# Performance work log

Measured on AMD Instinct MI355X. Metric: run time of the kernel, lower is better.

The kernel has to match this reference:

```python
import jax, jax.numpy as jnp
import numpy as np

H = 512
IN = 64
OUT = 1


def _lstm_layer(x, W_ih, W_hh, b_ih, b_hh):
    # x: (B, T, D). PyTorch gate order: i, f, g, o stacked along 4H.
    B, T, _ = x.shape
    Hd = W_hh.shape[1]
    # Precompute input contribution for all timesteps (one big GEMM).
    xg = jnp.einsum('btd,gd->btg', x, W_ih) + b_ih + b_hh  # (B, T, 4H)

    def step(carry, xg_t):
        h, c = carry
        gates = xg_t + h @ W_hh.T  # (B, 4H)
        i, f, g, o = jnp.split(gates, 4, axis=-1)
        i = jax.nn.sigmoid(i)
        f = jax.nn.sigmoid(f)
        g = jnp.tanh(g)
        o = jax.nn.sigmoid(o)
        c = f * c + i * g
        h = o * jnp.tanh(c)
        return (h, c), h

    h0 = jnp.zeros((B, Hd), x.dtype)
    c0 = jnp.zeros((B, Hd), x.dtype)
    (_, _), hs = jax.lax.scan(step, (h0, c0), jnp.swapaxes(xg, 0, 1))
    return jnp.swapaxes(hs, 0, 1)  # (B, T, H)


def setup_inputs() -> dict:
    key = jax.random.key(0)
    ks = jax.random.split(key, 12)
    s = 1.0 / np.sqrt(H)  # PyTorch LSTM init scale
    u = lambda k, shp: jax.random.uniform(k, shp, jnp.float32, -s, s)
    return {
        'x': jax.random.normal(ks[0], (64, 512, IN), jnp.float32),
        'W_ih0': u(ks[1], (4 * H, IN)),
        'W_hh0': u(ks[2], (4 * H, H)),
        'b_ih0': u(ks[3], (4 * H,)),
        'b_hh0': u(ks[4], (4 * H,)),
        'W_ih1': u(ks[5], (4 * H, H)),
        'W_hh1': u(ks[6], (4 * H, H)),
        'b_ih1': u(ks[7], (4 * H,)),
        'b_hh1': u(ks[8], (4 * H,)),
        'fc_w': u(ks[9], (OUT, H)),
        'fc_b': u(ks[10], (OUT,)),
    }


def reference(x, W_ih0, W_hh0, b_ih0, b_hh0, W_ih1, W_hh1, b_ih1, b_hh1, fc_w, fc_b):
    # Two stacked LSTM layers (eval mode: inter-layer dropout disabled),
    # then linear head on the last timestep's hidden state.
    h1 = _lstm_layer(x, W_ih0, W_hh0, b_ih0, b_hh0)   # (B, T, H)
    h2 = _lstm_layer(h1, W_ih1, W_hh1, b_ih1, b_hh1)  # (B, T, H)
    return h2[:, -1, :] @ fc_w.T + fc_b               # (B, OUT)
```

## Files before the change

### kernel.cpp

```cpp
#include <hip/hip_runtime.h>
#include <stdint.h>

static constexpr int NBLK = 256;
static constexpr int NTHR = 256;
static constexpr int Hd   = 512;
static constexpr int Td   = 512;
static constexpr int IND  = 64;
static constexpr int Bd   = 64;
static constexpr int HBUF = Bd * Hd;
static constexpr int HR   = 520;
static constexpr unsigned POIS32 = 0xAAAAAAAAu;

typedef __attribute__((ext_vector_type(8))) short short8;
typedef __attribute__((ext_vector_type(4))) float f4;

#define MFMA(a, b, c) __builtin_amdgcn_mfma_f32_16x16x32_bf16((a), (b), (c), 0, 0, 0)

__device__ __forceinline__ uint64_t ld_agent64(const uint64_t* p) {
  return __hip_atomic_load((uint64_t*)p, __ATOMIC_RELAXED, __HIP_MEMORY_SCOPE_AGENT);
}
__device__ __forceinline__ void st_agent32(unsigned* p, unsigned v) {
  __hip_atomic_store(p, v, __ATOMIC_RELAXED, __HIP_MEMORY_SCOPE_AGENT);
}
__device__ __forceinline__ float sigmoidf_(float v) { return 1.0f / (1.0f + __expf(-v)); }
__device__ __forceinline__ float tanhf_(float v) {
  v = fminf(15.0f, fmaxf(-15.0f, v));
  float e = __expf(2.0f * v);
  return (e - 1.0f) / (e + 1.0f);
}
__device__ __forceinline__ unsigned short bf16_rne(float f) {
  unsigned u = __float_as_uint(f);
  unsigned r = u + 0x7FFFu + ((u >> 16) & 1u);
  return (unsigned short)(r >> 16);
}
__device__ __forceinline__ unsigned pack_h(float h) {
  unsigned short hb = bf16_rne(h);
  float hf = __uint_as_float((unsigned)hb << 16);
  unsigned short lb = bf16_rne(h - hf);
  unsigned pk = ((unsigned)hb << 16) | (unsigned)lb;
  if (pk == POIS32) pk ^= 1u;
  return pk;
}
__device__ __forceinline__ int good64(uint64_t w) {
  return (int)((unsigned)w != POIS32) & (int)((unsigned)(w >> 32) != POIS32);
}
__device__ __forceinline__ void spin_check16(const uint64_t* base, int tid, uint64_t* tmp) {
  int guard = 0;
  for (;;) {
    unsigned ok = 1;
    #pragma unroll
    for (int k = 0; k < 16; ++k) ok &= (unsigned)good64(tmp[k]);
    if (ok || ++guard > (1 << 16)) break;
    __builtin_amdgcn_s_sleep(1);
    #pragma unroll
    for (int k = 0; k < 16; ++k) tmp[k] = ld_agent64(base + k * 256 + tid);
  }
}
__device__ __forceinline__ void load_split8(const float* src, short8* hi, short8* lo) {
  float wv[8];
  *(float4*)&wv[0] = *(const float4*)src;
  *(float4*)&wv[4] = *(const float4*)(src + 4);
  #pragma unroll
  for (int j = 0; j < 8; ++j) {
    unsigned short hb = bf16_rne(wv[j]);
    float r = wv[j] - __uint_as_float((unsigned)hb << 16);
    ((short*)hi)[j] = (short)hb;
    ((short*)lo)[j] = (short)bf16_rne(r);
  }
}

__global__ __launch_bounds__(256) void split_x_kernel(
    const float* __restrict__ x, short* __restrict__ xhi, short* __restrict__ xlo) {
  int i = blockIdx.x * 256 + threadIdx.x;
  float4 v = ((const float4*)x)[i];
  float f[4] = {v.x, v.y, v.z, v.w};
  unsigned h[4], l[4];
  #pragma unroll
  for (int e = 0; e < 4; ++e) {
    unsigned short hb = bf16_rne(f[e]);
    float r = f[e] - __uint_as_float((unsigned)hb << 16);
    h[e] = hb; l[e] = bf16_rne(r);
  }
  uint2 hp = {h[0] | (h[1] << 16), h[2] | (h[3] << 16)};
  uint2 lp = {l[0] | (l[1] << 16), l[2] | (l[3] << 16)};
  *(uint2*)&xhi[i * 4] = hp;
  *(uint2*)&xlo[i * 4] = lp;
}

__global__ __launch_bounds__(NTHR, 1) void lstm2_flow(
    const float* __restrict__ Wih0, const float* __restrict__ Whh0,
    const float* __restrict__ bih0, const float* __restrict__ bhh0,
    const float* __restrict__ Wih1, const float* __restrict__ Whh1,
    const float* __restrict__ bih1, const float* __restrict__ bhh1,
    const float* __restrict__ fcw,  const float* __restrict__ fcb,
    float* __restrict__ out,
    const short* __restrict__ xhi, const short* __restrict__ xlo,
    unsigned* __restrict__ h1, unsigned* __restrict__ h2)
{
  __shared__ short hiA1[16 * HR];
  __shared__ short loA1[16 * HR];
  __shared__ short hiA2[16 * HR];
  __shared__ short loA2[16 * HR];
  __shared__ short Blo[4 * 16 * 64 * 8];
  __shared__ float gp[4][4][16][17];
  __shared__ float red[NTHR];

  const int tid  = threadIdx.x;
  const int wave = tid >> 6;
  const int lane = tid & 63;
  const int nB   = lane & 15;
  const int q    = lane >> 4;
  const int mA   = lane & 15;

  const int xcd   = blockIdx.x & 7;
  const int layer = xcd >> 2;
  const int mt    = xcd & 3;
  const int jt    = blockIdx.x >> 3;
  const int jBase = jt * 16;
  const int bBase = mt * 16;

  const int pm = tid >> 4;
  const int pn = tid & 15;

  if (layer == 0) {
    short8 bhhh[4][4], bhhl[4][4];
    short8 bxh[4], bxl[4];
    #pragma unroll
    for (int g = 0; g < 4; ++g) {
      #pragma unroll
      for (int kk = 0; kk < 4; ++kk) {
        const float* src = Whh0 + (size_t)(g * Hd + jBase + nB) * Hd + (wave * 4 + kk) * 32 + q * 8;
        load_split8(src, &bhhh[g][kk], &bhhl[g][kk]);
      }
    }
    if (wave < 2) {
      #pragma unroll
      for (int g = 0; g < 4; ++g) {
        const float* src = Wih0 + (size_t)(g * Hd + jBase + nB) * IND + wave * 32 + q * 8;
        load_split8(src, &bxh[g], &bxl[g]);
      }
    }
    float bias[4];
    #pragma unroll
    for (int g4 = 0; g4 < 4; ++g4) {
      int r = g4 * Hd + jBase + pn;
      bias[g4] = bih0[r] + bhh0[r];
    }
    float c1 = 0.0f;

    for (int t = 0; t < Td; ++t) {
      const uint64_t* s1 = (const uint64_t*)(h1 + (size_t)((t >= 1) ? t - 1 : 0) * HBUF)
                           + bBase * 256;
      uint64_t tmp[16];
      if (t >= 1) {
        #pragma unroll
        for (int k = 0; k < 16; ++k) tmp[k] = ld_agent64(s1 + k * 256 + tid);
      }

      f4 aH[4] = {{0.f,0.f,0.f,0.f},{0.f,0.f,0.f,0.f},{0.f,0.f,0.f,0.f},{0.f,0.f,0.f,0.f}};
      f4 aL[4] = {{0.f,0.f,0.f,0.f},{0.f,0.f,0.f,0.f},{0.f,0.f,0.f,0.f},{0.f,0.f,0.f,0.f}};

      if (wave < 2) {
        const size_t xb = ((size_t)(bBase + mA) * Td + t) * IND + wave * 32 + q * 8;
        short8 xh = *(const short8*)&xhi[xb];
        short8 xl = *(const short8*)&xlo[xb];
        #pragma unroll
        for (int g = 0; g < 4; ++g) {
          aH[g] = MFMA(xh, bxh[g], aH[g]);
          aL[g] = MFMA(xh, bxl[g], aL[g]);
          aL[g] = MFMA(xl, bxh[g], aL[g]);
        }
      }

      if (t >= 1) {
        spin_check16(s1, tid, tmp);
        #pragma unroll
        for (int k = 0; k < 16; ++k) {
          unsigned p0 = (unsigned)tmp[k], p1 = (unsigned)(tmp[k] >> 32);
          *(unsigned*)&hiA1[k * HR + tid * 2] = __builtin_amdgcn_perm(p1, p0, 0x07060302u);
          *(unsigned*)&loA1[k * HR + tid * 2] = __builtin_amdgcn_perm(p1, p0, 0x05040100u);
        }
        #pragma unroll
        for (int kk = 0; kk < 4; ++kk) {
          const int kt = wave * 4 + kk;
          short8 ah = *(const short8*)&hiA1[mA * HR + kt * 32 + q * 8];
          short8 al = *(const short8*)&loA1[mA * HR + kt * 32 + q * 8];
          #pragma unroll
          for (int g = 0; g < 4; ++g) {
            aH[g] = MFMA(ah, bhhh[g][kk], aH[g]);
            aL[g] = MFMA(ah, bhhl[g][kk], aL[g]);
            aL[g] = MFMA(al, bhhh[g][kk], aL[g]);
          }
        }
      }
      #pragma unroll
      for (int g = 0; g < 4; ++g) {
        #pragma unroll
        for (int r2 = 0; r2 < 4; ++r2)
          gp[wave][g][q * 4 + r2][nB] = aH[g][r2] + aL[g][r2];
      }
      __syncthreads();

      {
        float pi = bias[0], pf = bias[1], pg = bias[2], po = bias[3];
        #pragma unroll
        for (int w = 0; w < 4; ++w) {
          pi += gp[w][0][pm][pn];
          pf += gp[w][1][pm][pn];
          pg += gp[w][2][pm][pn];
          po += gp[w][3][pm][pn];
        }
        float ig = sigmoidf_(pi), fg = sigmoidf_(pf), gg = tanhf_(pg), og = sigmoidf_(po);
        c1 = fmaf(fg, c1, ig * gg);
        float h = og * tanhf_(c1);
        st_agent32(h1 + (size_t)t * HBUF + (bBase + pm) * Hd + jBase + pn, pack_h(h));
      }
      __syncthreads();
    }

    if (blockIdx.x == 0) {
      const int b = tid >> 2, q4 = tid & 3;
      float sum = 0.0f;
      #pragma unroll
      for (int ch = 0; ch < 4; ++ch) {
        const uint64_t* hp = (const uint64_t*)(h2 + (size_t)(Td - 1) * HBUF) + b * 256 + q4 * 64 + ch * 16;
        uint64_t w[16];
        int guard = 0;
        for (;;) {
          unsigned ok = 1;
          #pragma unroll
          for (int u = 0; u < 16; ++u) w[u] = ld_agent64(hp + u);
          #pragma unroll
          for (int u = 0; u < 16; ++u) ok &= (unsigned)good64(w[u]);
          if (ok || ++guard > (1 << 17)) break;
          __builtin_amdgcn_s_sleep(1);
        }
        #pragma unroll
        for (int u = 0; u < 16; ++u) {
          int cw = q4 * 64 + ch * 16 + u;
          unsigned plo = (unsigned)w[u], phi = (unsigned)(w[u] >> 32);
          float vlo = __uint_as_float(plo & 0xFFFF0000u) + __uint_as_float(plo << 16);
          float vhi = __uint_as_float(phi & 0xFFFF0000u) + __uint_as_float(phi << 16);
          sum = fmaf(vlo, fcw[2 * cw], fmaf(vhi, fcw[2 * cw + 1], sum));
        }
      }
      red[tid] = sum;
      __syncthreads();
      if (q4 == 0) out[b] = red[tid] + red[tid + 1] + red[tid + 2] + red[tid + 3] + fcb[0];
    }
  } else {
    short8 bihh[4][4], bihl[4][4], bhhh[4][4];
    #pragma unroll
    for (int g = 0; g < 4; ++g) {
      #pragma unroll
      for (int kk = 0; kk < 4; ++kk) {
        const int kt = wave * 4 + kk;
        const float* srcI = Wih1 + (size_t)(g * Hd + jBase + nB) * Hd + kt * 32 + q * 8;
        load_split8(srcI, &bihh[g][kk], &bihl[g][kk]);
        const float* srcH = Whh1 + (size_t)(g * Hd + jBase + nB) * Hd + kt * 32 + q * 8;
        short8 hlo;
        load_split8(srcH, &bhhh[g][kk], &hlo);
        *(short8*)&Blo[((g * 16 + kt) * 64 + lane) * 8] = hlo;
      }
    }
    float bias[4];
    #pragma unroll
    for (int g4 = 0; g4 < 4; ++g4) {
      int r = g4 * Hd + jBase + pn;
      bias[g4] = bih1[r] + bhh1[r];
    }
    float c2 = 0.0f;
    __syncthreads();

    for (int t = 0; t < Td; ++t) {
      const uint64_t* s1 = (const uint64_t*)(h1 + (size_t)t * HBUF) + bBase * 256;
      const uint64_t* s2 = (const uint64_t*)(h2 + (size_t)((t >= 1) ? t - 1 : 0) * HBUF)
                           + bBase * 256;
      uint64_t t1[16], t2[16];
      #pragma unroll
      for (int k = 0; k < 16; ++k) t1[k] = ld_agent64(s1 + k * 256 + tid);
      if (t >= 1) {
        #pragma unroll
        for (int k = 0; k < 16; ++k) t2[k] = ld_agent64(s2 + k * 256 + tid);
      }

      f4 aH[4] = {{0.f,0.f,0.f,0.f},{0.f,0.f,0.f,0.f},{0.f,0.f,0.f,0.f},{0.f,0.f,0.f,0.f}};
      f4 aL[4] = {{0.f,0.f,0.f,0.f},{0.f,0.f,0.f,0.f},{0.f,0.f,0.f,0.f},{0.f,0.f,0.f,0.f}};

      spin_check16(s1, tid, t1);
      #pragma unroll
      for (int k = 0; k < 16; ++k) {
        unsigned p0 = (unsigned)t1[k], p1 = (unsigned)(t1[k] >> 32);
        *(unsigned*)&hiA1[k * HR + tid * 2] = __builtin_amdgcn_perm(p1, p0, 0x07060302u);
        *(unsigned*)&loA1[k * HR + tid * 2] = __builtin_amdgcn_perm(p1, p0, 0x05040100u);
      }
      #pragma unroll
      for (int kk = 0; kk < 4; ++kk) {
        const int kt = wave * 4 + kk;
        short8 ah = *(const short8*)&hiA1[mA * HR + kt * 32 + q * 8];
        short8 al = *(const short8*)&loA1[mA * HR + kt * 32 + q * 8];
        #pragma unroll
        for (int g = 0; g < 4; ++g) {
          aH[g] = MFMA(ah, bihh[g][kk], aH[g]);
          aL[g] = MFMA(ah, bihl[g][kk], aL[g]);
          aL[g] = MFMA(al, bihh[g][kk], aL[g]);
        }
      }
      if (t >= 1) {
        spin_check16(s2, tid, t2);
        #pragma unroll
        for (int k = 0; k < 16; ++k) {
          unsigned q0 = (unsigned)t2[k], q1 = (unsigned)(t2[k] >> 32);
          *(unsigned*)&hiA2[k * HR + tid * 2] = __builtin_amdgcn_perm(q1, q0, 0x07060302u);
          *(unsigned*)&loA2[k * HR + tid * 2] = __builtin_amdgcn_perm(q1, q0, 0x05040100u);
        }
        #pragma unroll
        for (int kk = 0; kk < 4; ++kk) {
          const int kt = wave * 4 + kk;
          short8 ah = *(const short8*)&hiA2[mA * HR + kt * 32 + q * 8];
          short8 al = *(const short8*)&loA2[mA * HR + kt * 32 + q * 8];
          #pragma unroll
          for (int g = 0; g < 4; ++g) {
            short8 wlo = *(const short8*)&Blo[((g * 16 + kt) * 64 + lane) * 8];
            aH[g] = MFMA(ah, bhhh[g][kk], aH[g]);
            aL[g] = MFMA(ah, wlo, aL[g]);
            aL[g] = MFMA(al, bhhh[g][kk], aL[g]);
          }
        }
      }
      #pragma unroll
      for (int g = 0; g < 4; ++g) {
        #pragma unroll
        for (int r2 = 0; r2 < 4; ++r2)
          gp[wave][g][q * 4 + r2][nB] = aH[g][r2] + aL[g][r2];
      }
      __syncthreads();

      {
        float pi = bias[0], pf = bias[1], pg = bias[2], po = bias[3];
        #pragma unroll
        for (int w = 0; w < 4; ++w) {
          pi += gp[w][0][pm][pn];
          pf += gp[w][1][pm][pn];
          pg += gp[w][2][pm][pn];
          po += gp[w][3][pm][pn];
        }
        float ig = sigmoidf_(pi), fg = sigmoidf_(pf), gg = tanhf_(pg), og = sigmoidf_(po);
        c2 = fmaf(fg, c2, ig * gg);
        float h = og * tanhf_(c2);
        st_agent32(h2 + (size_t)t * HBUF + (bBase + pm) * Hd + jBase + pn, pack_h(h));
      }
      __syncthreads();
    }
  }
}

extern "C" void kernel_launch(void* const* d_in, const int* in_sizes, int n_in,
                              void* d_out, int out_size, void* d_ws, size_t ws_size,
                              hipStream_t stream) {
  const float* x    = (const float*)d_in[0];
  const float* Wih0 = (const float*)d_in[1];
  const float* Whh0 = (const float*)d_in[2];
  const float* bih0 = (const float*)d_in[3];
  const float* bhh0 = (const float*)d_in[4];
  const float* Wih1 = (const float*)d_in[5];
  const float* Whh1 = (const float*)d_in[6];
  const float* bih1 = (const float*)d_in[7];
  const float* bhh1 = (const float*)d_in[8];
  const float* fcw  = (const float*)d_in[9];
  const float* fcb  = (const float*)d_in[10];

  char* base = (char*)d_ws;
  short* xhi = (short*)base;
  const size_t xplane = (size_t)Bd * Td * IND;
  short* xlo = xhi + xplane;
  unsigned* h1 = (unsigned*)(xlo + xplane);
  unsigned* h2 = h1 + (size_t)Td * HBUF;

  const size_t need = 4 * xplane + 2 * (size_t)Td * HBUF * 4;
  if (ws_size < need) return;

  hipLaunchKernelGGL(split_x_kernel, dim3((unsigned)(xplane / 4 / 256)), dim3(256), 0, stream,
                     x, xhi, xlo);
  hipLaunchKernelGGL(lstm2_flow, dim3(NBLK), dim3(NTHR), 0, stream,
                     Wih0, Whh0, bih0, bhh0, Wih1, Whh1, bih1, bhh1, fcw, fcb,
                     (float*)d_out, xhi, xlo, h1, h2);
}
```

Baseline: 2.159 ms.

## Store hidden state in MFMA fragment layout and drop LDS staging

Hidden states are now written to global memory in a layout that matches the MFMA A-operand fragments. Each lane reads its own 4x64-bit words directly, polls them in chunks of four, and unpacks them in registers, so the LDS staging buffers, their writes and their reads are gone. The gate partial-sum buffer is double-buffered by timestep parity, which removes the second __syncthreads per step. The finer-grained spins let MFMA work on early k-chunks start before the whole vector has arrived. The cost is scattered, less coalesced global loads and stores per lane.

```diff
diff --git a/kernel.cpp b/kernel.cpp
--- a/kernel.cpp
+++ b/kernel.cpp
@@ -8,8 +8,8 @@
 static constexpr int IND  = 64;
 static constexpr int Bd   = 64;
 static constexpr int HBUF = Bd * Hd;
-static constexpr int HR   = 520;
 static constexpr unsigned POIS32 = 0xAAAAAAAAu;
+
 
 typedef __attribute__((ext_vector_type(8))) short short8;
 typedef __attribute__((ext_vector_type(4))) float f4;
@@ -44,17 +44,25 @@
 __device__ __forceinline__ int good64(uint64_t w) {
   return (int)((unsigned)w != POIS32) & (int)((unsigned)(w >> 32) != POIS32);
 }
-__device__ __forceinline__ void spin_check16(const uint64_t* base, int tid, uint64_t* tmp) {
+__device__ __forceinline__ void spin4(uint64_t* w, const uint64_t* p) {
   int guard = 0;
   for (;;) {
-    unsigned ok = 1;
-    #pragma unroll
-    for (int k = 0; k < 16; ++k) ok &= (unsigned)good64(tmp[k]);
+    unsigned ok = (unsigned)(good64(w[0]) & good64(w[1]) & good64(w[2]) & good64(w[3]));
     if (ok || ++guard > (1 << 16)) break;
     __builtin_amdgcn_s_sleep(1);
-    #pragma unroll
-    for (int k = 0; k < 16; ++k) tmp[k] = ld_agent64(base + k * 256 + tid);
-  }
+    w[0] = ld_agent64(p);     w[1] = ld_agent64(p + 1);
+    w[2] = ld_agent64(p + 2); w[3] = ld_agent64(p + 3);
+  }
+}
+__device__ __forceinline__ void unpack4(const uint64_t* w, short8* hi, short8* lo) {
+  union { unsigned u[4]; short8 s; } H, L;
+  #pragma unroll
+  for (int i = 0; i < 4; ++i) {
+    unsigned p0 = (unsigned)w[i], p1 = (unsigned)(w[i] >> 32);
+    H.u[i] = __builtin_amdgcn_perm(p1, p0, 0x07060302u);
+    L.u[i] = __builtin_amdgcn_perm(p1, p0, 0x05040100u);
+  }
+  *hi = H.s; *lo = L.s;
 }
 __device__ __forceinline__ void load_split8(const float* src, short8* hi, short8* lo) {
   float wv[8];
@@ -97,12 +105,8 @@
     const short* __restrict__ xhi, const short* __restrict__ xlo,
     unsigned* __restrict__ h1, unsigned* __restrict__ h2)
 {
-  __shared__ short hiA1[16 * HR];
-  __shared__ short loA1[16 * HR];
-  __shared__ short hiA2[16 * HR];
-  __shared__ short loA2[16 * HR];
   __shared__ short Blo[4 * 16 * 64 * 8];
-  __shared__ float gp[4][4][16][17];
+  __shared__ float gp[2][4][4][16][17];
   __shared__ float red[NTHR];
 
   const int tid  = threadIdx.x;
@@ -122,6 +126,13 @@
   const int pm = tid >> 4;
   const int pn = tid & 15;
 
+  unsigned offs[4];
+  #pragma unroll
+  for (int kk = 0; kk < 4; ++kk)
+    offs[kk] = (unsigned)((((wave * 4 + kk) * 4 + q) * 64 + bBase + mA) * 4);
+
+  const unsigned stIdx = (unsigned)((((jBase + pn) >> 3) * 64 + bBase + pm) * 8 + (pn & 7));
+
   if (layer == 0) {
     short8 bhhh[4][4], bhhl[4][4];
     short8 bxh[4], bxl[4];
@@ -149,12 +160,14 @@
     float c1 = 0.0f;
 
     for (int t = 0; t < Td; ++t) {
-      const uint64_t* s1 = (const uint64_t*)(h1 + (size_t)((t >= 1) ? t - 1 : 0) * HBUF)
-                           + bBase * 256;
+      const uint64_t* hp = (const uint64_t*)(h1 + (size_t)((t >= 1) ? t - 1 : 0) * HBUF);
       uint64_t tmp[16];
       if (t >= 1) {
         #pragma unroll
-        for (int k = 0; k < 16; ++k) tmp[k] = ld_agent64(s1 + k * 256 + tid);
+        for (int kk = 0; kk < 4; ++kk) {
+          #pragma unroll
+          for (int i = 0; i < 4; ++i) tmp[kk * 4 + i] = ld_agent64(hp + offs[kk] + i);
+        }
       }
 
       f4 aH[4] = {{0.f,0.f,0.f,0.f},{0.f,0.f,0.f,0.f},{0.f,0.f,0.f,0.f},{0.f,0.f,0.f,0.f}};
@@ -173,18 +186,11 @@
       }
 
       if (t >= 1) {
-        spin_check16(s1, tid, tmp);
-        #pragma unroll
-        for (int k = 0; k < 16; ++k) {
-          unsigned p0 = (unsigned)tmp[k], p1 = (unsigned)(tmp[k] >> 32);
-          *(unsigned*)&hiA1[k * HR + tid * 2] = __builtin_amdgcn_perm(p1, p0, 0x07060302u);
-          *(unsigned*)&loA1[k * HR + tid * 2] = __builtin_amdgcn_perm(p1, p0, 0x05040100u);
-        }
         #pragma unroll
         for (int kk = 0; kk < 4; ++kk) {
-          const int kt = wave * 4 + kk;
-          short8 ah = *(const short8*)&hiA1[mA * HR + kt * 32 + q * 8];
-          short8 al = *(const short8*)&loA1[mA * HR + kt * 32 + q * 8];
+          spin4(&tmp[kk * 4], hp + offs[kk]);
+          short8 ah, al;
+          unpack4(&tmp[kk * 4], &ah, &al);
           #pragma unroll
           for (int g = 0; g < 4; ++g) {
             aH[g] = MFMA(ah, bhhh[g][kk], aH[g]);
@@ -197,7 +203,7 @@
       for (int g = 0; g < 4; ++g) {
         #pragma unroll
         for (int r2 = 0; r2 < 4; ++r2)
-          gp[wave][g][q * 4 + r2][nB] = aH[g][r2] + aL[g][r2];
+          gp[t & 1][wave][g][q * 4 + r2][nB] = aH[g][r2] + aL[g][r2];
       }
       __syncthreads();
 
@@ -205,43 +211,36 @@
         float pi = bias[0], pf = bias[1], pg = bias[2], po = bias[3];
         #pragma unroll
         for (int w = 0; w < 4; ++w) {
-          pi += gp[w][0][pm][pn];
-          pf += gp[w][1][pm][pn];
-          pg += gp[w][2][pm][pn];
-          po += gp[w][3][pm][pn];
+          pi += gp[t & 1][w][0][pm][pn];
+          pf += gp[t & 1][w][1][pm][pn];
+          pg += gp[t & 1][w][2][pm][pn];
+          po += gp[t & 1][w][3][pm][pn];
         }
         float ig = sigmoidf_(pi), fg = sigmoidf_(pf), gg = tanhf_(pg), og = sigmoidf_(po);
         c1 = fmaf(fg, c1, ig * gg);
         float h = og * tanhf_(c1);
-        st_agent32(h1 + (size_t)t * HBUF + (bBase + pm) * Hd + jBase + pn, pack_h(h));
-      }
-      __syncthreads();
+        st_agent32(h1 + (size_t)t * HBUF + stIdx, pack_h(h));
+      }
     }
 
     if (blockIdx.x == 0) {
       const int b = tid >> 2, q4 = tid & 3;
       float sum = 0.0f;
-      #pragma unroll
-      for (int ch = 0; ch < 4; ++ch) {
-        const uint64_t* hp = (const uint64_t*)(h2 + (size_t)(Td - 1) * HBUF) + b * 256 + q4 * 64 + ch * 16;
-        uint64_t w[16];
-        int guard = 0;
-        for (;;) {
-          unsigned ok = 1;
-          #pragma unroll
-          for (int u = 0; u < 16; ++u) w[u] = ld_agent64(hp + u);
-          #pragma unroll
-          for (int u = 0; u < 16; ++u) ok &= (unsigned)good64(w[u]);
-          if (ok || ++guard > (1 << 17)) break;
-          __builtin_amdgcn_s_sleep(1);
-        }
-        #pragma unroll
-        for (int u = 0; u < 16; ++u) {
-          int cw = q4 * 64 + ch * 16 + u;
-          unsigned plo = (unsigned)w[u], phi = (unsigned)(w[u] >> 32);
+      const uint64_t* h2p = (const uint64_t*)(h2 + (size_t)(Td - 1) * HBUF);
+      for (int cb8 = 0; cb8 < 16; ++cb8) {
+        const int cb = q4 * 16 + cb8;
+        const uint64_t* p = h2p + (size_t)(cb * 64 + b) * 4;
+        uint64_t w4[4];
+        #pragma unroll
+        for (int i = 0; i < 4; ++i) w4[i] = ld_agent64(p + i);
+        spin4(w4, p);
+        #pragma unroll
+        for (int i2 = 0; i2 < 4; ++i2) {
+          int c0 = cb * 8 + 2 * i2;
+          unsigned plo = (unsigned)w4[i2], phi = (unsigned)(w4[i2] >> 32);
           float vlo = __uint_as_float(plo & 0xFFFF0000u) + __uint_as_float(plo << 16);
           float vhi = __uint_as_float(phi & 0xFFFF0000u) + __uint_as_float(phi << 16);
-          sum = fmaf(vlo, fcw[2 * cw], fmaf(vhi, fcw[2 * cw + 1], sum));
+          sum = fmaf(vlo, fcw[c0], fmaf(vhi, fcw[c0 + 1], sum));
         }
       }
       red[tid] = sum;
@@ -273,32 +272,30 @@
     __syncthreads();
 
     for (int t = 0; t < Td; ++t) {
-      const uint64_t* s1 = (const uint64_t*)(h1 + (size_t)t * HBUF) + bBase * 256;
-      const uint64_t* s2 = (const uint64_t*)(h2 + (size_t)((t >= 1) ? t - 1 : 0) * HBUF)
-                           + bBase * 256;
+      const uint64_t* hp1 = (const uint64_t*)(h1 + (size_t)t * HBUF);
+      const uint64_t* hp2 = (const uint64_t*)(h2 + (size_t)((t >= 1) ? t - 1 : 0) * HBUF);
       uint64_t t1[16], t2[16];
       #pragma unroll
-      for (int k = 0; k < 16; ++k) t1[k] = ld_agent64(s1 + k * 256 + tid);
+      for (int kk = 0; kk < 4; ++kk) {
+        #pragma unroll
+        for (int i = 0; i < 4; ++i) t1[kk * 4 + i] = ld_agent64(hp1 + offs[kk] + i);
+      }
       if (t >= 1) {
         #pragma unroll
-        for (int k = 0; k < 16; ++k) t2[k] = ld_agent64(s2 + k * 256 + tid);
+        for (int kk = 0; kk < 4; ++kk) {
+          #pragma unroll
+          for (int i = 0; i < 4; ++i) t2[kk * 4 + i] = ld_agent64(hp2 + offs[kk] + i);
+        }
       }
 
       f4 aH[4] = {{0.f,0.f,0.f,0.f},{0.f,0.f,0.f,0.f},{0.f,0.f,0.f,0.f},{0.f,0.f,0.f,0.f}};
       f4 aL[4] = {{0.f,0.f,0.f,0.f},{0.f,0.f,0.f,0.f},{0.f,0.f,0.f,0.f},{0.f,0.f,0.f,0.f}};
 
-      spin_check16(s1, tid, t1);
-      #pragma unroll
-      for (int k = 0; k < 16; ++k) {
-        unsigned p0 = (unsigned)t1[k], p1 = (unsigned)(t1[k] >> 32);
-        *(unsigned*)&hiA1[k * HR + tid * 2] = __builtin_amdgcn_perm(p1, p0, 0x07060302u);
-        *(unsigned*)&loA1[k * HR + tid * 2] = __builtin_amdgcn_perm(p1, p0, 0x05040100u);
-      }
       #pragma unroll
       for (int kk = 0; kk < 4; ++kk) {
-        const int kt = wave * 4 + kk;
-        short8 ah = *(const short8*)&hiA1[mA * HR + kt * 32 + q * 8];
-        short8 al = *(const short8*)&loA1[mA * HR + kt * 32 + q * 8];
+        spin4(&t1[kk * 4], hp1 + offs[kk]);
+        short8 ah, al;
+        unpack4(&t1[kk * 4], &ah, &al);
         #pragma unroll
         for (int g = 0; g < 4; ++g) {
           aH[g] = MFMA(ah, bihh[g][kk], aH[g]);
@@ -307,18 +304,12 @@
         }
       }
       if (t >= 1) {
-        spin_check16(s2, tid, t2);
-        #pragma unroll
-        for (int k = 0; k < 16; ++k) {
-          unsigned q0 = (unsigned)t2[k], q1 = (unsigned)(t2[k] >> 32);
-          *(unsigned*)&hiA2[k * HR + tid * 2] = __builtin_amdgcn_perm(q1, q0, 0x07060302u);
-          *(unsigned*)&loA2[k * HR + tid * 2] = __builtin_amdgcn_perm(q1, q0, 0x05040100u);
-        }
         #pragma unroll
         for (int kk = 0; kk < 4; ++kk) {
+          spin4(&t2[kk * 4], hp2 + offs[kk]);
+          short8 ah, al;
+          unpack4(&t2[kk * 4], &ah, &al);
           const int kt = wave * 4 + kk;
-          short8 ah = *(const short8*)&hiA2[mA * HR + kt * 32 + q * 8];
-          short8 al = *(const short8*)&loA2[mA * HR + kt * 32 + q * 8];
           #pragma unroll
           for (int g = 0; g < 4; ++g) {
             short8 wlo = *(const short8*)&Blo[((g * 16 + kt) * 64 + lane) * 8];
@@ -332,7 +323,7 @@
       for (int g = 0; g < 4; ++g) {
         #pragma unroll
         for (int r2 = 0; r2 < 4; ++r2)
-          gp[wave][g][q * 4 + r2][nB] = aH[g][r2] + aL[g][r2];
+          gp[t & 1][wave][g][q * 4 + r2][nB] = aH[g][r2] + aL[g][r2];
       }
       __syncthreads();
 
@@ -340,17 +331,16 @@
         float pi = bias[0], pf = bias[1], pg = bias[2], po = bias[3];
         #pragma unroll
         for (int w = 0; w < 4; ++w) {
-          pi += gp[w][0][pm][pn];
-          pf += gp[w][1][pm][pn];
-          pg += gp[w][2][pm][pn];
-          po += gp[w][3][pm][pn];
+          pi += gp[t & 1][w][0][pm][pn];
+          pf += gp[t & 1][w][1][pm][pn];
+          pg += gp[t & 1][w][2][pm][pn];
+          po += gp[t & 1][w][3][pm][pn];
         }
         float ig = sigmoidf_(pi), fg = sigmoidf_(pf), gg = tanhf_(pg), og = sigmoidf_(po);
         c2 = fmaf(fg, c2, ig * gg);
         float h = og * tanhf_(c2);
-        st_agent32(h2 + (size_t)t * HBUF + (bBase + pm) * Hd + jBase + pn, pack_h(h));
-      }
-      __syncthreads();
+        st_agent32(h2 + (size_t)t * HBUF + stIdx, pack_h(h));
+      }
     }
   }
 }
```

Result: slower. 2.986 ms (+38.3%).
